# Kernel tuning notes

Measured on AMD Instinct MI355X. Metric: run time of the kernel, lower is better.

## Reference

```python
import jax, jax.numpy as jnp
import numpy as np

N_NODES, N_EDGES, N_PAIRS, FEAT, N_LAYERS = 10000, 160000, 8, 64, 2


def setup_inputs() -> dict:
    key = jax.random.key(0)
    ks = jax.random.split(key, 12)
    s = 1.0 / np.sqrt(FEAT)
    x = jax.random.normal(ks[0], (N_NODES, FEAT), jnp.float32)
    # distinct node ids so unique(pos) has exactly 2*N_PAIRS elements (static B)
    pos = jax.random.permutation(ks[1], N_NODES)[: 2 * N_PAIRS].reshape(N_PAIRS, 2).astype(jnp.int32)
    edge_src = jax.random.randint(ks[2], (N_EDGES,), 0, N_NODES, jnp.int32)
    edge_dst = jax.random.randint(ks[3], (N_EDGES,), 0, N_NODES, jnp.int32)
    edge_weight = jax.random.uniform(ks[4], (N_EDGES,), jnp.float32)
    f0_w = jax.random.normal(ks[5], (N_LAYERS, FEAT, FEAT), jnp.float32) * s
    f0_b = jax.random.normal(ks[6], (N_LAYERS, FEAT), jnp.float32) * 0.01
    f1_w = jax.random.normal(ks[7], (N_LAYERS, FEAT, FEAT), jnp.float32) * s
    f1_b = jax.random.normal(ks[8], (N_LAYERS, FEAT), jnp.float32) * 0.01
    conv_w = jax.random.normal(ks[9], (N_LAYERS, FEAT, FEAT), jnp.float32) * s
    conv_b = jax.random.normal(ks[10], (N_LAYERS, FEAT), jnp.float32) * 0.01
    return {"x": x, "pos": pos, "edge_src": edge_src, "edge_dst": edge_dst,
            "edge_weight": edge_weight, "f0_w": f0_w, "f0_b": f0_b,
            "f1_w": f1_w, "f1_b": f1_b, "conv_w": conv_w, "conv_b": conv_b}


def reference(x, pos, edge_src, edge_dst, edge_weight, f0_w, f0_b, f1_w, f1_b, conv_w, conv_b):
    N = x.shape[0]
    M = pos.shape[0]
    B = 2 * M  # pos entries are distinct -> B unique labeled nodes (static)
    L = f0_w.shape[0]
    # convert_pos: sel_id = unique labeled nodes, ret = flat index into (B*N)
    sel_id, inv = jnp.unique(pos, return_inverse=True, size=B, fill_value=0)
    inv = inv.reshape(pos.shape)
    ret = pos + inv[:, ::-1] * N  # (M,2): pair (u,v) -> x0[batch_of_v, u], x0[batch_of_u, v]
    idx0 = jnp.arange(B)

    h = x  # layer 0: (N,F); later layers: (B,N,H)
    for i in range(L):
        if i == 0:
            base = h @ f0_w[0] + f0_b[0]                         # (N,H)
            x0 = jnp.broadcast_to(base, (B,) + base.shape)       # (B,N,H)
            x1 = h[sel_id] @ f1_w[0] + f1_b[0]                   # (B,H)
        else:
            x0 = h @ f0_w[i] + f0_b[i]                           # (B,N,H)
            x1 = h[idx0, sel_id] @ f1_w[i] + f1_b[i]             # (B,H)
        x0 = x0.at[idx0, sel_id].set(x1)  # scatter labeled-node embeddings
        # sparse adjacency conv: aggregate over edges, then linear
        xT = jnp.swapaxes(x0, 0, 1)                              # (N,B,H)
        msgs = xT[edge_src] * edge_weight[:, None, None]         # (E,B,H)
        agg = jax.ops.segment_sum(msgs, edge_dst, num_segments=N)  # (N,B,H)
        h = jnp.swapaxes(agg, 0, 1) @ conv_w[i] + conv_b[i]      # (B,N,H)
        if i < L - 1:
            h = jax.nn.relu(h)
    flat = h.reshape(B * N, -1)
    return flat[ret]  # (M, 2, H)
```

## Files before the change

### kernel.cpp

```cpp
#include <hip/hip_runtime.h>

#define F 64
#define SECAP 8192
#define TCAP 2048
#define FCAP 8256
#define BLK 256
#define EPIW 4

struct Params {
  const float *x, *ew, *f0w, *f0b, *f1w, *f1b, *cw, *cb;
  const int *pos, *esrc, *edst;
  float *out;
  int B, E;
  int *cnt;
  int *TEn;
  unsigned *bitmap;
  int *sel, *slotb, *slot_of, *SEb, *SEd, *TEsrc2;
  float *SEw, *TEw2, *AGG, *wsum, *zf;
  float *P0, *G, *V, *Wp;
  float *b0c, *gb, *vb, *wpb;
  int4 *zbase;
  int nzvec;
};

#define MVB(res, init, vecp, mat)                         \
  {                                                       \
    float a0_ = 0.f, a1_ = 0.f, a2_ = 0.f, a3_ = 0.f;     \
    _Pragma("unroll")                                     \
    for (int q_ = 0; q_ < 16; ++q_) {                     \
      float4 vv_ = ((const float4*)(vecp))[q_];           \
      a0_ += vv_.x * (mat)[(4 * q_ + 0) * 64 + h];        \
      a1_ += vv_.y * (mat)[(4 * q_ + 1) * 64 + h];        \
      a2_ += vv_.z * (mat)[(4 * q_ + 2) * 64 + h];        \
      a3_ += vv_.w * (mat)[(4 * q_ + 3) * 64 + h];        \
    }                                                     \
    res = (init) + ((a0_ + a1_) + (a2_ + a3_));           \
  }

__global__ __launch_bounds__(BLK) void kp_pre(Params p) {
  const int tid = threadIdx.x;
  const int bid = blockIdx.x;
  if (bid < 2) {
    for (int i = bid * BLK + tid; i < p.nzvec; i += 2 * BLK)
      p.zbase[i] = make_int4(0, 0, 0, 0);
    return;
  }
  __shared__ __align__(16) float Al[64][64];
  const int ty = tid >> 6, h = tid & 63;
  if (bid < 6) {
    int wb = bid - 2;
    const float *A, *A2 = nullptr, *Bm;
    float* Om;
    if (wb == 0)      { A = p.f0w;        Bm = p.cw;        Om = p.P0; }
    else if (wb == 1) { A = p.f1w;        A2 = p.f0w; Bm = p.cw; Om = p.G; }
    else if (wb == 2) { A = p.f1w + 4096; Bm = p.cw + 4096; Om = p.V; }
    else              { A = p.f0w + 4096; Bm = p.cw + 4096; Om = p.Wp; }
    for (int i = tid; i < 4096; i += BLK)
      Al[i >> 6][i & 63] = A2 ? (A[i] - A2[i]) : A[i];
    __syncthreads();
    float acc[16];
#pragma unroll
    for (int fi = 0; fi < 16; ++fi) acc[fi] = 0.f;
    for (int k = 0; k < 64; ++k) {
      float bkh = Bm[k * 64 + h];
#pragma unroll
      for (int fi = 0; fi < 16; ++fi)
        acc[fi] += Al[ty * 16 + fi][k] * bkh;
    }
#pragma unroll
    for (int fi = 0; fi < 16; ++fi)
      Om[(ty * 16 + fi) * 64 + h] = acc[fi];
  } else {
    const float *vsrc, *v2 = nullptr, *Bm;
    float* Ov;
    if (ty == 0)      { vsrc = p.f0b;      Bm = p.cw;        Ov = p.b0c; }
    else if (ty == 1) { vsrc = p.f1b;      v2 = p.f0b; Bm = p.cw; Ov = p.gb; }
    else if (ty == 2) { vsrc = p.f1b + 64; Bm = p.cw + 4096; Ov = p.vb; }
    else              { vsrc = p.f0b + 64; Bm = p.cw + 4096; Ov = p.wpb; }
    Al[ty][h] = v2 ? (vsrc[h] - v2[h]) : vsrc[h];
    float acc;
    MVB(acc, 0.f, Al[ty], Bm);
    Ov[h] = acc;
  }
}

__device__ __forceinline__ void mark_assign(const Params& p, int n) {
  unsigned bit = 1u << (n & 31);
  unsigned old = atomicOr(&p.bitmap[n >> 5], bit);
  if (!(old & bit)) {
    int sl = atomicAdd(&p.cnt[2], 1);
    if (sl < FCAP) {
      p.slot_of[n] = sl;
      float4* row = (float4*)(p.AGG + (size_t)sl * F);
#pragma unroll
      for (int k = 0; k < 16; ++k) row[k] = make_float4(0.f, 0.f, 0.f, 0.f);
      p.wsum[sl] = 0.f;
    } else {
      p.slot_of[n] = 0;
    }
  }
}

__global__ __launch_bounds__(BLK) void kp_scan(Params p) {
  __shared__ int posL[16], rankL[16];
  const int tid = threadIdx.x;
  const int B = p.B;
  if (tid < B) {
    int v = p.pos[tid];
    int rank = 0;
    for (int j = 0; j < B; ++j) rank += (p.pos[j] < v);
    posL[tid] = v;
    rankL[tid] = rank;
  }
  __syncthreads();
  if (blockIdx.x == 0 && tid < B) {
    p.sel[rankL[tid]] = posL[tid];
    p.slotb[tid] = rankL[tid ^ 1];
    mark_assign(p, posL[tid]);
  }
  int gtid = blockIdx.x * BLK + tid;
  int nthr = gridDim.x * BLK;
  for (int e = gtid; e < p.E; e += nthr) {
    int s = p.esrc[e], d = p.edst[e];
    float w = p.ew[e];
    int bi = -1, ti = -1;
#pragma unroll
    for (int j = 0; j < 16; ++j) {
      if (j < B) {
        if (s == posL[j]) bi = rankL[j];
        if (d == posL[j]) ti = j;
      }
    }
    if (bi >= 0) {
      int idx = atomicAdd(&p.cnt[0], 1);
      if (idx < SECAP) { p.SEb[idx] = bi; p.SEd[idx] = d; p.SEw[idx] = w; }
    }
    if (ti >= 0) {
      int idx = atomicAdd(&p.TEn[ti], 1);
      if (idx < TCAP) { p.TEsrc2[ti * TCAP + idx] = s; p.TEw2[ti * TCAP + idx] = w; }
      mark_assign(p, s);
    }
  }
}

__global__ __launch_bounds__(BLK) void kp_agg(Params p) {
  int gtid = blockIdx.x * BLK + threadIdx.x;
  int nthr = gridDim.x * BLK;
  for (int e = gtid; e < p.E; e += nthr) {
    int d = p.edst[e];
    if (!((p.bitmap[d >> 5] >> (d & 31)) & 1u)) continue;
    int sl = p.slot_of[d];
    if ((unsigned)sl >= (unsigned)FCAP) continue;
    int s = p.esrc[e];
    float w = p.ew[e];
    const float4* xs = (const float4*)(p.x + (size_t)s * F);
    float* dst = p.AGG + (size_t)sl * F;
#pragma unroll
    for (int k = 0; k < 16; ++k) {
      float4 v = xs[k];
      atomicAdd(dst + 4 * k + 0, w * v.x);
      atomicAdd(dst + 4 * k + 1, w * v.y);
      atomicAdd(dst + 4 * k + 2, w * v.z);
      atomicAdd(dst + 4 * k + 3, w * v.w);
    }
    atomicAdd(&p.wsum[sl], w);
  }
}

__global__ __launch_bounds__(BLK) void kp_zf(Params p) {
  __shared__ __align__(16) float a[4][64];
  const int Fn = min(p.cnt[2], FCAP);
  const int ty = threadIdx.x >> 6, h = threadIdx.x & 63;
  for (int sl = blockIdx.x * 4 + ty; sl < Fn; sl += gridDim.x * 4) {
    a[ty][h] = p.AGG[(size_t)sl * F + h];
    float z;
    MVB(z, p.wsum[sl] * p.b0c[h] + p.cb[h], a[ty], p.P0);
    p.zf[(size_t)sl * F + h] = z;
  }
}

__global__ __launch_bounds__(BLK) void kp_epi(Params p) {
  __shared__ float cL[FCAP];
  __shared__ __align__(16) float v0[EPIW][64];
  __shared__ __align__(16) float Sp[EPIW][64];
  __shared__ float wnsL[EPIW], wselL[EPIW];
  __shared__ int slL[TCAP];
  __shared__ float twL[TCAP];
  const int t = blockIdx.x;
  const int tid = threadIdx.x;
  const int h = tid & 63, wv = tid >> 6;
  const int b = p.slotb[t];
  const int seln = p.sel[b];
  const int Fn = min(p.cnt[2], FCAP);
  for (int i = tid; i < Fn; i += BLK) cL[i] = 0.f;
  __syncthreads();
  int sen = min(p.cnt[0], SECAP);
  for (int i = tid; i < sen; i += BLK) {
    if (p.SEb[i] == b) {
      int d = p.SEd[i];
      if ((p.bitmap[d >> 5] >> (d & 31)) & 1u) {
        int sl = p.slot_of[d];
        if ((unsigned)sl < (unsigned)FCAP) atomicAdd(&cL[sl], p.SEw[i]);
      }
    }
  }
  int ten = min(p.TEn[t], TCAP);
  for (int i = tid; i < ten; i += BLK) {
    int s = p.TEsrc2[t * TCAP + i];
    int sl;
    if (s == seln) sl = -1;
    else { sl = p.slot_of[s]; if ((unsigned)sl >= (unsigned)FCAP) sl = 0; }
    slL[i] = sl;
    twL[i] = p.TEw2[t * TCAP + i];
  }
  __syncthreads();
  v0[wv][h] = p.x[(size_t)seln * F + h];
  float g0h;
  MVB(g0h, p.gb[h], v0[wv], p.G);
  int sslot = p.slot_of[seln];
  if ((unsigned)sslot >= (unsigned)FCAP) sslot = 0;
  float h1self = fmaxf(p.zf[(size_t)sslot * F + h] + cL[sslot] * g0h, 0.f);
  v0[wv][h] = h1self;
  float x11Th;
  MVB(x11Th, p.vb[h], v0[wv], p.V);
  float S = 0.f, wns = 0.f, wsel = 0.f;
  for (int i = wv; i < ten; i += EPIW) {
    int sl = slL[i];
    float w = twL[i];
    if (sl < 0) { wsel += w; continue; }
    float h1 = fmaxf(p.zf[(size_t)sl * F + h] + cL[sl] * g0h, 0.f);
    S += w * h1;
    wns += w;
  }
  Sp[wv][h] = S;
  if (h == 0) { wnsL[wv] = wns; wselL[wv] = wsel; }
  __syncthreads();
  if (wv == 0) {
    float Sh = Sp[0][h] + Sp[1][h] + Sp[2][h] + Sp[3][h];
    float wnsT = wnsL[0] + wnsL[1] + wnsL[2] + wnsL[3];
    float wselT = wselL[0] + wselL[1] + wselL[2] + wselL[3];
    v0[0][h] = Sh;
    float o;
    MVB(o, wnsT * p.wpb[h] + wselT * x11Th + p.cb[64 + h], v0[0], p.Wp);
    p.out[t * F + h] = o;
  }
}

extern "C" void kernel_launch(void* const* d_in, const int* in_sizes, int n_in,
                              void* d_out, int out_size, void* d_ws, size_t ws_size,
                              hipStream_t stream) {
  Params hp;
  hp.x = (const float*)d_in[0];
  hp.pos = (const int*)d_in[1];
  hp.esrc = (const int*)d_in[2];
  hp.edst = (const int*)d_in[3];
  hp.ew = (const float*)d_in[4];
  hp.f0w = (const float*)d_in[5];
  hp.f0b = (const float*)d_in[6];
  hp.f1w = (const float*)d_in[7];
  hp.f1b = (const float*)d_in[8];
  hp.cw = (const float*)d_in[9];
  hp.cb = (const float*)d_in[10];
  hp.out = (float*)d_out;
  const int N = in_sizes[0] / F;
  hp.B = in_sizes[1];
  hp.E = in_sizes[2];

  char* w = (char*)d_ws;
  size_t off = 0;
  auto take = [&](size_t nb) { size_t r = off; off += (nb + 255) & ~(size_t)255; return r; };
  size_t o_cnt = take(256);
  size_t o_ten = take(256);
  size_t o_bitmap = take(((size_t)N + 31) / 32 * 4);
  size_t zero_end = off;
  size_t o_sel = take(256);
  size_t o_slotb = take(256);
  size_t o_slotof = take((size_t)N * 4);
  size_t o_seb = take(SECAP * 4);
  size_t o_sed = take(SECAP * 4);
  size_t o_sew = take(SECAP * 4);
  size_t o_tesrc = take((size_t)hp.B * TCAP * 4);
  size_t o_tew = take((size_t)hp.B * TCAP * 4);
  size_t o_agg = take((size_t)FCAP * F * 4);
  size_t o_wsum = take((size_t)FCAP * 4);
  size_t o_zf = take((size_t)FCAP * F * 4);
  size_t o_P0 = take(4096 * 4);
  size_t o_G = take(4096 * 4);
  size_t o_V = take(4096 * 4);
  size_t o_Wp = take(4096 * 4);
  size_t o_b0c = take(256);
  size_t o_gb = take(256);
  size_t o_vb = take(256);
  size_t o_wpb = take(256);
  (void)ws_size;

  hp.cnt = (int*)(w + o_cnt);
  hp.TEn = (int*)(w + o_ten);
  hp.bitmap = (unsigned*)(w + o_bitmap);
  hp.sel = (int*)(w + o_sel);
  hp.slotb = (int*)(w + o_slotb);
  hp.slot_of = (int*)(w + o_slotof);
  hp.SEb = (int*)(w + o_seb);
  hp.SEd = (int*)(w + o_sed);
  hp.SEw = (float*)(w + o_sew);
  hp.TEsrc2 = (int*)(w + o_tesrc);
  hp.TEw2 = (float*)(w + o_tew);
  hp.AGG = (float*)(w + o_agg);
  hp.wsum = (float*)(w + o_wsum);
  hp.zf = (float*)(w + o_zf);
  hp.P0 = (float*)(w + o_P0);
  hp.G = (float*)(w + o_G);
  hp.V = (float*)(w + o_V);
  hp.Wp = (float*)(w + o_Wp);
  hp.b0c = (float*)(w + o_b0c);
  hp.gb = (float*)(w + o_gb);
  hp.vb = (float*)(w + o_vb);
  hp.wpb = (float*)(w + o_wpb);
  hp.zbase = (int4*)w;
  hp.nzvec = (int)(zero_end / 16);

  kp_pre<<<7, BLK, 0, stream>>>(hp);
  int nbE = (hp.E + BLK - 1) / BLK;
  if (nbE > 2048) nbE = 2048;
  kp_scan<<<nbE, BLK, 0, stream>>>(hp);
  kp_agg<<<nbE, BLK, 0, stream>>>(hp);
  kp_zf<<<128, BLK, 0, stream>>>(hp);
  kp_epi<<<hp.B, BLK, 0, stream>>>(hp);
  (void)n_in; (void)out_size;
}
```

Measured before the change: 59.48 us.

## Fuse the frontier linear transform into the epilogue kernel and drop kp_zf

Removes the separate kp_zf launch that applied P0 to every frontier slot's aggregate. Instead each epilogue block computes only the rows it needs. Three of its four wavefronts compute up to ZCAP neighbor rows into a shared buffer, while wavefront 0 handles the self row. This saves one kernel launch and the zf global round trip. In exchange it may redo row transforms when blocks share slots, adds a block sync, and uses more shared memory (48KB zbuf plus cL), which may lower occupancy.

```diff
diff --git a/kernel.cpp b/kernel.cpp
--- a/kernel.cpp
+++ b/kernel.cpp
@@ -6,6 +6,7 @@
 #define FCAP 8256
 #define BLK 256
 #define EPIW 4
+#define ZCAP 192
 
 struct Params {
   const float *x, *ew, *f0w, *f0b, *f1w, *f1b, *cw, *cb;
@@ -16,7 +17,7 @@
   int *TEn;
   unsigned *bitmap;
   int *sel, *slotb, *slot_of, *SEb, *SEd, *TEsrc2;
-  float *SEw, *TEw2, *AGG, *wsum, *zf;
+  float *SEw, *TEw2, *AGG, *wsum;
   float *P0, *G, *V, *Wp;
   float *b0c, *gb, *vb, *wpb;
   int4 *zbase;
@@ -167,20 +168,12 @@
   }
 }
 
-__global__ __launch_bounds__(BLK) void kp_zf(Params p) {
-  __shared__ __align__(16) float a[4][64];
-  const int Fn = min(p.cnt[2], FCAP);
-  const int ty = threadIdx.x >> 6, h = threadIdx.x & 63;
-  for (int sl = blockIdx.x * 4 + ty; sl < Fn; sl += gridDim.x * 4) {
-    a[ty][h] = p.AGG[(size_t)sl * F + h];
-    float z;
-    MVB(z, p.wsum[sl] * p.b0c[h] + p.cb[h], a[ty], p.P0);
-    p.zf[(size_t)sl * F + h] = z;
-  }
-}
+#define ZROW(res, sl)                                                     \
+  MVB(res, p.wsum[sl] * p.b0c[h] + p.cb[h], (p.AGG + (size_t)(sl) * F), p.P0)
 
 __global__ __launch_bounds__(BLK) void kp_epi(Params p) {
   __shared__ float cL[FCAP];
+  __shared__ __align__(16) float zbuf[ZCAP][64];
   __shared__ __align__(16) float v0[EPIW][64];
   __shared__ __align__(16) float Sp[EPIW][64];
   __shared__ float wnsL[EPIW], wselL[EPIW];
@@ -219,16 +212,33 @@
   MVB(g0h, p.gb[h], v0[wv], p.G);
   int sslot = p.slot_of[seln];
   if ((unsigned)sslot >= (unsigned)FCAP) sslot = 0;
-  float h1self = fmaxf(p.zf[(size_t)sslot * F + h] + cL[sslot] * g0h, 0.f);
-  v0[wv][h] = h1self;
-  float x11Th;
-  MVB(x11Th, p.vb[h], v0[wv], p.V);
+  float x11Th = 0.f;
+  if (wv == 0) {
+    float zs;
+    ZROW(zs, sslot);
+    float h1self = fmaxf(zs + cL[sslot] * g0h, 0.f);
+    v0[0][h] = h1self;
+    MVB(x11Th, p.vb[h], v0[0], p.V);
+  } else {
+    int zmax = min(ten, ZCAP);
+    for (int i = wv - 1; i < zmax; i += EPIW - 1) {
+      int sl = slL[i];
+      if (sl < 0) continue;
+      float z;
+      ZROW(z, sl);
+      zbuf[i][h] = z;
+    }
+  }
+  __syncthreads();
   float S = 0.f, wns = 0.f, wsel = 0.f;
   for (int i = wv; i < ten; i += EPIW) {
     int sl = slL[i];
     float w = twL[i];
     if (sl < 0) { wsel += w; continue; }
-    float h1 = fmaxf(p.zf[(size_t)sl * F + h] + cL[sl] * g0h, 0.f);
+    float zv;
+    if (i < ZCAP) zv = zbuf[i][h];
+    else ZROW(zv, sl);
+    float h1 = fmaxf(zv + cL[sl] * g0h, 0.f);
     S += w * h1;
     wns += w;
   }
@@ -283,7 +293,6 @@
   size_t o_tew = take((size_t)hp.B * TCAP * 4);
   size_t o_agg = take((size_t)FCAP * F * 4);
   size_t o_wsum = take((size_t)FCAP * 4);
-  size_t o_zf = take((size_t)FCAP * F * 4);
   size_t o_P0 = take(4096 * 4);
   size_t o_G = take(4096 * 4);
   size_t o_V = take(4096 * 4);
@@ -307,7 +316,6 @@
   hp.TEw2 = (float*)(w + o_tew);
   hp.AGG = (float*)(w + o_agg);
   hp.wsum = (float*)(w + o_wsum);
-  hp.zf = (float*)(w + o_zf);
   hp.P0 = (float*)(w + o_P0);
   hp.G = (float*)(w + o_G);
   hp.V = (float*)(w + o_V);
@@ -324,7 +332,6 @@
   if (nbE > 2048) nbE = 2048;
   kp_scan<<<nbE, BLK, 0, stream>>>(hp);
   kp_agg<<<nbE, BLK, 0, stream>>>(hp);
-  kp_zf<<<128, BLK, 0, stream>>>(hp);
   kp_epi<<<hp.B, BLK, 0, stream>>>(hp);
   (void)n_in; (void)out_size;
 }
```

New measurement: 59.82 us. Within noise of the previous version (+0.6%).
